# Optimization experiments

Hardware: AMD Instinct MI355X
Metric: run time of the kernel (lower is better)

The kernel has to match this reference:

```python
import jax, jax.numpy as jnp
import numpy as np

V = 30000   # vocab (from get_word_embedding default)
D = 640     # d_model
L = 6       # num_layers
H = 8       # num_heads
DH = D // H # head dim 80
FF = 4 * D  # ffn hidden 2560
BOS = 1
EOS = 2
LN_EPS = 1e-6


def _ln(x, s, b):
    m = x.mean(-1, keepdims=True)
    v = ((x - m) ** 2).mean(-1, keepdims=True)
    return (x - m) / jnp.sqrt(v + LN_EPS) * s + b


def _get_logits(tokens, seq_len, emb, Wq, bq, Wk, bk, Wv, bv, Wo, bo,
                ln1s, ln1b, W1, b1, W2, b2, ln2s, ln2b, lmW, lmb):
    # tokens: (B,S) int; seq_len: (B,) int
    B, S = tokens.shape
    h = emb[tokens]                                   # (B,S,D), no pos-enc / scaling in source
    look_ahead = jnp.triu(jnp.ones((S, S), jnp.float32), k=1)          # 1 = masked (TF-style)
    pad = (jnp.arange(S)[None, :] >= seq_len[:, None]).astype(jnp.float32)  # (B,S)
    mask = jnp.maximum(look_ahead[None, None, :, :], pad[:, None, None, :])  # (B,1,S,S)

    def layer(h, p):
        wq, bq_, wk, bk_, wv, bv_, wo, bo_, l1s, l1b, w1, b1_, w2, b2_, l2s, l2b = p
        q = (h @ wq + bq_).reshape(B, S, H, DH)
        k = (h @ wk + bk_).reshape(B, S, H, DH)
        v = (h @ wv + bv_).reshape(B, S, H, DH)
        scores = jnp.einsum('bqhd,bkhd->bhqk', q, k) / jnp.sqrt(jnp.float32(DH))
        scores = scores - mask * 1e9
        a = jax.nn.softmax(scores, axis=-1)
        o = jnp.einsum('bhqk,bkhd->bqhd', a, v).reshape(B, S, D) @ wo + bo_
        h = _ln(h + o, l1s, l1b)                      # post-LN residual
        f = jax.nn.relu(h @ w1 + b1_) @ w2 + b2_
        h = _ln(h + f, l2s, l2b)
        return h, None

    h, _ = jax.lax.scan(layer, h, (Wq, bq, Wk, bk, Wv, bv, Wo, bo,
                                   ln1s, ln1b, W1, b1, W2, b2, ln2s, ln2b))
    return h @ lmW + lmb                              # (B,S,V)


def setup_inputs() -> dict:
    key = jax.random.key(0)
    ks = jax.random.split(key, 12)
    std = 0.02

    def n(k, shape):
        return jax.random.normal(k, shape, jnp.float32) * std

    return {
        'initial_words': jax.random.randint(ks[0], (4, 8), 3, V, dtype=jnp.int32),
        'max_length': 32,
        'emb': n(ks[1], (V, D)),
        'Wq': n(ks[2], (L, D, D)), 'bq': jnp.zeros((L, D), jnp.float32),
        'Wk': n(ks[3], (L, D, D)), 'bk': jnp.zeros((L, D), jnp.float32),
        'Wv': n(ks[4], (L, D, D)), 'bv': jnp.zeros((L, D), jnp.float32),
        'Wo': n(ks[5], (L, D, D)), 'bo': jnp.zeros((L, D), jnp.float32),
        'ln1s': jnp.ones((L, D), jnp.float32), 'ln1b': jnp.zeros((L, D), jnp.float32),
        'W1': n(ks[6], (L, D, FF)), 'b1': jnp.zeros((L, FF), jnp.float32),
        'W2': n(ks[7], (L, FF, D)), 'b2': jnp.zeros((L, D), jnp.float32),
        'ln2s': jnp.ones((L, D), jnp.float32), 'ln2b': jnp.zeros((L, D), jnp.float32),
        'lmW': n(ks[8], (D, V)), 'lmb': jnp.zeros((V,), jnp.float32),
    }


def reference(initial_words, max_length, emb, Wq, bq, Wk, bk, Wv, bv, Wo, bo,
              ln1s, ln1b, W1, b1, W2, b2, ln2s, ln2b, lmW, lmb):
    B, init_len = initial_words.shape
    seq_len = jnp.full((B,), max_length, jnp.int32)
    S = max_length + 1  # BOS + max_length slots, as in the torch padding logic
    inp = (jnp.zeros((B, S), jnp.int32)
           .at[:, 0].set(BOS)
           .at[:, 1:1 + init_len].set(initial_words.astype(jnp.int32)))

    def cond(c):
        _inp, cl, tok = c
        return (cl + 1 <= max_length) & jnp.any(tok != EOS)

    def body(c):
        inp, cl, _tok = c
        logits = _get_logits(inp, seq_len, emb, Wq, bq, Wk, bk, Wv, bv, Wo, bo,
                             ln1s, ln1b, W1, b1, W2, b2, ln2s, ln2b, lmW, lmb)
        step_logits = jax.lax.dynamic_index_in_dim(logits, cl, axis=1, keepdims=False)
        tok = jnp.argmax(step_logits, axis=-1).astype(jnp.int32)
        inp = inp.at[:, cl + 1].set(tok)
        return (inp, cl + 1, tok)

    inp, _, _ = jax.lax.while_loop(
        cond, body,
        (inp, jnp.int32(init_len), jnp.full((B,), -100, jnp.int32)))
    return inp[:, 1:]
```

## Files before the change

kernel.cpp:

```cpp
#include <hip/hip_runtime.h>
#include <math.h>

#define B 4
#define SEQ 33
#define MAXLEN 32
#define D 640
#define NH 8
#define DH 80
#define NL 6
#define FF 2560
#define V 30000
#define INITLEN 8
#define NBLK 1024
#define NT 256
#define EOS_TOK 2
#define NPOS_P 9
#define NR_P 36
#define LM_NB 938

#define QKV_N 240
#define AW_B 240
#define AW_E 304
#define F1_B 304
#define F1_E 624
#define F2_B 624
#define F2_E 784

#define NFLAGS 1024
#define NSLOT 32
#define SLOT_U 16

#define VER(t,l) ((size_t)((t) * NL + (l)))

typedef float f4 __attribute__((ext_vector_type(4)));

struct Par {
  const int* iw;
  const float* emb;
  const float *Wq, *bq, *Wk, *bk, *Wv, *bv, *Wo, *bo;
  const float *ln1s, *ln1b, *W1, *b1, *W2, *b2, *ln2s, *ln2b, *lmW, *lmb;
  int* out;
};

__device__ __align__(256) float g_Kc[(size_t)NL * B * NH * SEQ * DH];
__device__ __align__(256) float g_Vc[(size_t)NL * B * NH * SEQ * DH];
__device__ __align__(256) float g_xv[(size_t)SEQ * NL * 2560];
__device__ __align__(256) float g_h1v[(size_t)SEQ * NL * 2560];
__device__ __align__(256) float g_qv[(size_t)SEQ * NL * 2560];
__device__ __align__(256) float g_opartv[(size_t)SEQ * NL * 20480];
__device__ __align__(256) float g_f1v[(size_t)SEQ * NL * 10240];
__device__ __align__(256) float g_f2v[(size_t)SEQ * NL * 5120];
__device__ __align__(256) float g_xlm[(size_t)SEQ * 2560];
__device__ __align__(256) int   g_tokv[SEQ * 64];
__device__ __align__(256) int   g_stopv[SEQ * 64];
__device__ float g_xp[NR_P * D];
__device__ float g_h1p[NR_P * D];
__device__ float g_qkvpP[(size_t)8 * 1920 * NR_P];
__device__ float g_qP[(size_t)NH * NR_P * DH];
__device__ float g_opartP[(size_t)NH * D * NR_P];
__device__ float g_f1pP[(size_t)8 * FF * NR_P];
__device__ float g_f2pP[(size_t)32 * D * NR_P];
__device__ unsigned long long g_keys[(size_t)NBLK * B];
__device__ int g_tokens[B * SEQ];
__device__ unsigned g_flags[(size_t)NFLAGS * NSLOT * SLOT_U];
__device__ unsigned g_arrive = 0;
__device__ unsigned g_gen = 0;

#define KCIDX(l,b,h,pos,j) (((((size_t)(l)*B+(b))*NH+(h))*SEQ+(pos))*DH+(j))

__device__ __forceinline__ float ldc(const float* p) {
  return __hip_atomic_load(p, __ATOMIC_RELAXED, __HIP_MEMORY_SCOPE_AGENT);
}
__device__ __forceinline__ void stc(float* p, float v) {
  __hip_atomic_store(p, v, __ATOMIC_RELAXED, __HIP_MEMORY_SCOPE_AGENT);
}
__device__ __forceinline__ int ldci(const int* p) {
  return __hip_atomic_load(p, __ATOMIC_RELAXED, __HIP_MEMORY_SCOPE_AGENT);
}
__device__ __forceinline__ void stci(int* p, int v) {
  __hip_atomic_store(p, v, __ATOMIC_RELAXED, __HIP_MEMORY_SCOPE_AGENT);
}
__device__ __forceinline__ void stcu64(unsigned long long* p, unsigned long long v) {
  __hip_atomic_store(p, v, __ATOMIC_RELAXED, __HIP_MEMORY_SCOPE_AGENT);
}
__device__ __forceinline__ void st4c(float* p, f4 v) {
  asm volatile("global_store_dwordx4 %0, %1, off sc1" :: "v"(p), "v"(v) : "memory");
}
__device__ __forceinline__ void ld4c_issue(f4& dst, const float* p) {
  asm volatile("global_load_dwordx4 %0, %1, off sc1" : "=v"(dst) : "v"(p) : "memory");
}
__device__ __forceinline__ void wait_vm() {
  asm volatile("s_waitcnt vmcnt(0)" ::: "memory");
  __builtin_amdgcn_sched_barrier(0);
}
__device__ __forceinline__ unsigned long long mk64(float lo, float hi) {
  return ((unsigned long long)__float_as_uint(hi) << 32) | (unsigned long long)__float_as_uint(lo);
}

__device__ __forceinline__ void gsync_full() {
  __syncthreads();
  if (threadIdx.x == 0) {
    __threadfence();
    unsigned g = __hip_atomic_load(&g_gen, __ATOMIC_SEQ_CST, __HIP_MEMORY_SCOPE_AGENT);
    unsigned old = __hip_atomic_fetch_add(&g_arrive, 1u, __ATOMIC_SEQ_CST, __HIP_MEMORY_SCOPE_AGENT);
    if (old == NBLK - 1u) {
      __hip_atomic_store(&g_arrive, 0u, __ATOMIC_SEQ_CST, __HIP_MEMORY_SCOPE_AGENT);
      __hip_atomic_fetch_add(&g_gen, 1u, __ATOMIC_SEQ_CST, __HIP_MEMORY_SCOPE_AGENT);
    } else {
      while (__hip_atomic_load(&g_gen, __ATOMIC_RELAXED, __HIP_MEMORY_SCOPE_AGENT) == g)
        __builtin_amdgcn_s_sleep(2);
    }
    __threadfence();
  }
  __syncthreads();
}

__device__ __forceinline__ void stage_done(int idx) {
  asm volatile("s_waitcnt vmcnt(0)" ::: "memory");
  __syncthreads();
  if (threadIdx.x == 0) {
    __hip_atomic_fetch_add(
        &g_flags[((size_t)idx * NSLOT + (blockIdx.x & (NSLOT - 1))) * SLOT_U],
        1u, __ATOMIC_RELAXED, __HIP_MEMORY_SCOPE_AGENT);
  }
}

__device__ __forceinline__ void stage_wait(int idx, unsigned cnt) {
  if (threadIdx.x < 64) {
    const unsigned* base = &g_flags[(size_t)idx * NSLOT * SLOT_U];
    int spins = 0;
    for (;;) {
      unsigned v = 0u;
      if (threadIdx.x < NSLOT)
        v = __hip_atomic_load(base + (size_t)threadIdx.x * SLOT_U,
                              __ATOMIC_RELAXED, __HIP_MEMORY_SCOPE_AGENT);
      #pragma unroll
      for (int o = 16; o > 0; o >>= 1) v += __shfl_down(v, o, 64);
      v = __shfl(v, 0, 64);
      if (v >= cnt) break;
      if (spins < 16)       __builtin_amdgcn_s_sleep(1);
      else if (spins < 128) __builtin_amdgcn_s_sleep(8);
      else                  __builtin_amdgcn_s_sleep(32);
      ++spins;
    }
  }
  __syncthreads();
  asm volatile("" ::: "memory");
}

__device__ __forceinline__ float bred_sum(float v, float* s_red) {
  #pragma unroll
  for (int o = 32; o > 0; o >>= 1) v += __shfl_down(v, o, 64);
  __syncthreads();
  if ((threadIdx.x & 63) == 0) s_red[threadIdx.x >> 6] = v;
  __syncthreads();
  return s_red[0] + s_red[1] + s_red[2] + s_red[3];
}

__device__ void ln_inplace(float* row, const float* gam, const float* bet, float* s_red) {
  float ps = 0.f;
  for (int d = threadIdx.x; d < D; d += NT) ps += row[d];
  const float m = bred_sum(ps, s_red) * (1.0f / 640.0f);
  float pv = 0.f;
  for (int d = threadIdx.x; d < D; d += NT) { float t = row[d] - m; pv += t * t; }
  const float var = bred_sum(pv, s_red) * (1.0f / 640.0f);
  const float rstd = 1.0f / sqrtf(var + 1e-6f);
  for (int d = threadIdx.x; d < D; d += NT)
    row[d] = (row[d] - m) * rstd * gam[d] + bet[d];
  __syncthreads();
}

__device__ __forceinline__ void ln_wave(float* s_x, const float* gam, const float* bet) {
  const int tid = threadIdx.x, w = tid >> 6, lane = tid & 63;
  float ps = 0.f;
  for (int i = lane; i < D; i += 64) ps += s_x[w * 640 + i];
  #pragma unroll
  for (int o = 32; o > 0; o >>= 1) ps += __shfl_xor(ps, o, 64);
  const float mean = ps * (1.0f / 640.0f);
  float pv = 0.f;
  for (int i = lane; i < D; i += 64) { float d = s_x[w * 640 + i] - mean; pv += d * d; }
  #pragma unroll
  for (int o = 32; o > 0; o >>= 1) pv += __shfl_xor(pv, o, 64);
  const float rstd = 1.0f / sqrtf(pv * (1.0f / 640.0f) + 1e-6f);
  for (int i = lane; i < D; i += 64)
    s_x[w * 640 + i] = (s_x[w * 640 + i] - mean) * rstd * gam[i] + bet[i];
}

__device__ __forceinline__ void build_x2w(const Par& p, int t, int lsrc, float* s_x) {
  const int tid = threadIdx.x, w = tid >> 6, lane = tid & 63;
  const size_t ver = VER(t, lsrc);
  const float* h1 = g_h1v + ver * 2560 + w * 640;
  const float* fa = g_f2v + ver * 5120 + w * 640;
  const float* fb = g_f2v + ver * 5120 + 2560 + w * 640;
  const float* b2 = p.b2 + (size_t)lsrc * D;
  for (int c4 = lane; c4 < 160; c4 += 64) {
    f4 a = *(const f4*)&h1[c4 * 4];
    f4 b = *(const f4*)&fa[c4 * 4];
    f4 c = *(const f4*)&fb[c4 * 4];
    const float* bb = b2 + c4 * 4;
    f4 s = { a.x + b.x + c.x + bb[0], a.y + b.y + c.y + bb[1],
             a.z + b.z + c.z + bb[2], a.w + b.w + c.w + bb[3] };
    *(f4*)&s_x[w * 640 + c4 * 4] = s;
  }
  ln_wave(s_x, p.ln2s + (size_t)lsrc * D, p.ln2b + (size_t)lsrc * D);
}


__device__ void st_QKV(const Par& p, int l, int t, float* s_x, float* s_t, float* s_r) {
  const int tid = threadIdx.x;
  const int cg = (blockIdx.x & 7) * 30 + (blockIdx.x >> 3);
  const int m = cg / 80, colm0 = (cg % 80) * 8;
  const int w = tid >> 6, lane = tid & 63;
  if (l == 0) {
    const int tok = g_tokv[t * 64 + w];
    for (int c4 = lane; c4 < 160; c4 += 64)
      *(f4*)&s_x[w * 640 + c4 * 4] = *(const f4*)&p.emb[(size_t)tok * D + c4 * 4];
  } else {
    build_x2w(p, t, l - 1, s_x);
  }
  __syncthreads();
  if (cg == 0) {
    const size_t xo = VER(t, l) * 2560;
    for (int i = tid; i < 640; i += NT)
      st4c(&g_xv[xo + (size_t)i * 4], *(f4*)&s_x[i * 4]);
  }
  const int ds = tid >> 3, c = tid & 7;
  const float* Wb = (m == 0 ? p.Wq : m == 1 ? p.Wk : p.Wv)
                    + (size_t)l * D * D + colm0 + c;
  float a0 = 0, a1 = 0, a2 = 0, a3 = 0;
  {
    float wv[20];
    #pragma unroll
    for (int j = 0; j < 20; ++j) wv[j] = Wb[(size_t)(ds + j * 32) * D];
    #pragma unroll
    for (int j = 0; j < 20; ++j) {
      const int dd = ds + j * 32;
      a0 = fmaf(s_x[dd],        wv[j], a0);
      a1 = fmaf(s_x[640 + dd],  wv[j], a1);
      a2 = fmaf(s_x[1280 + dd], wv[j], a2);
      a3 = fmaf(s_x[1920 + dd], wv[j], a3);
    }
  }
  { f4 av = { a0, a1, a2, a3 }; *(f4*)&s_t[c * 132 + ds * 4] = av; }
  __syncthreads();
  if (tid < 32) {
    const int c2 = tid >> 2, b = tid & 3;
    float v = 0.f;
    #pragma unroll
    for (int d2 = 0; d2 < 32; ++d2) v += s_t[c2 * 132 + d2 * 4 + b];
    v += (m == 0 ? p.bq : m == 1 ? p.bk : p.bv)[(size_t)l * D + colm0 + c2];
    s_r[c2 * 4 + b] = v;
  }
  __syncthreads();
  if (m == 0) {
    if (tid < 8) {
      f4 v = { s_r[tid * 4], s_r[tid * 4 + 1], s_r[tid * 4 + 2], s_r[tid * 4 + 3] };
      st4c(&g_qv[VER(t, l) * 2560 + (size_t)(colm0 + tid) * 4], v);
    }
  } else {
    const int h = colm0 / 80, j0 = colm0 % 80;
    if (tid < 8) {
      const int b = tid >> 1, cq4 = (tid & 1) * 4;
      f4 v = { s_r[(cq4+0)*4+b], s_r[(cq4+1)*4+b], s_r[(cq4+2)*4+b], s_r[(cq4+3)*4+b] };
      float* cache = (m == 1) ? g_Kc : g_Vc;
      st4c(&cache[KCIDX(l, b, h, t, j0 + cq4)], v);
    }
  }
}

__device__ void st_AW(const Par& p, int l, int t,
                      float* s_q, float* s_sc, float* s_o, float* s_wo) {
  const int idx = blockIdx.x - AW_B, h = idx >> 3, c = idx & 7, tid = threadIdx.x;
  const size_t qo = VER(t, l) * 2560;
  if (tid < 80) {
    f4 q = *(const f4*)&g_qv[qo + (size_t)(h * 80 + tid) * 4];
    s_q[tid] = q.x; s_q[80 + tid] = q.y; s_q[160 + tid] = q.z; s_q[240 + tid] = q.w;
  }
  __syncthreads();
  const int nk = t + 1;
  for (int task = tid; task < 4 * nk; task += NT) {
    const int b = task / nk, kp = task % nk;
    const float* qq = s_q + b * 80;
    const f4* kk = (const f4*)&g_Kc[KCIDX(l, b, h, kp, 0)];
    float sd = 0.f;
    #pragma unroll
    for (int j4 = 0; j4 < 20; ++j4) {
      f4 k4 = kk[j4];
      sd += qq[j4*4+0]*k4.x + qq[j4*4+1]*k4.y + qq[j4*4+2]*k4.z + qq[j4*4+3]*k4.w;
    }
    s_sc[b * 33 + kp] = sd / 8.94427190999915878564f;
  }
  __syncthreads();
  if (tid < 4) {
    const int b = tid;
    float m = -1e30f;
    for (int k = 0; k < nk; ++k) m = fmaxf(m, s_sc[b * 33 + k]);
    float sum = 0.f;
    for (int k = 0; k < nk; ++k) { float e = expf(s_sc[b * 33 + k] - m); s_sc[b * 33 + k] = e; sum += e; }
    s_sc[132 + b] = 1.0f / sum;
  }
  __syncthreads();
  if (tid < 80) {
    const int b = tid / 20, j4 = tid % 20;
    f4 acc = { 0.f, 0.f, 0.f, 0.f };
    for (int kp = 0; kp < nk; ++kp) {
      f4 v = *(const f4*)&g_Vc[KCIDX(l, b, h, kp, j4 * 4)];
      const float wgt = s_sc[b * 33 + kp];
      acc.x += wgt * v.x; acc.y += wgt * v.y; acc.z += wgt * v.z; acc.w += wgt * v.w;
    }
    const float r = s_sc[132 + b];
    f4 o = { acc.x * r, acc.y * r, acc.z * r, acc.w * r };
    *(f4*)&s_o[b * 80 + j4 * 4] = o;
  }
  __syncthreads();
  if (tid < 240) {
    const int j = tid % 80, sub = tid / 80;
    const int col = c * 80 + j;
    const int d0 = sub * 27, d1 = (sub == 2) ? 80 : d0 + 27;
    const float* Wo = p.Wo + (size_t)l * D * D + col;
    float a0 = 0, a1 = 0, a2 = 0, a3 = 0;
    #pragma unroll 9
    for (int dd = d0; dd < d1; ++dd) {
      const float w = Wo[(size_t)(h * 80 + dd) * D];
      a0 += s_o[0*80+dd] * w; a1 += s_o[80+dd] * w;
      a2 += s_o[160+dd] * w; a3 += s_o[240+dd] * w;
    }
    float* tp = s_wo + (j * 3 + sub) * 4;
    tp[0] = a0; tp[1] = a1; tp[2] = a2; tp[3] = a3;
  }
  __syncthreads();
  if (tid < 80) {
    const int b = tid / 20, cq = tid % 20;
    f4 v;
    #pragma unroll
    for (int i = 0; i < 4; ++i) {
      const int j = cq * 4 + i;
      v[i] = s_wo[(j*3+0)*4+b] + s_wo[(j*3+1)*4+b] + s_wo[(j*3+2)*4+b];
    }
    st4c(&g_opartv[VER(t, l) * 20480 + (size_t)(h * 4 + b) * 640 + c * 80 + cq * 4], v);
  }
}

__device__ void st_F1(const Par& p, int l, int t, float* s_x, float* s_t, float* s_r) {
  const int tid = threadIdx.x;
  const int raw = blockIdx.x - F1_B;
  const int cg = (raw & 7) * 40 + (raw >> 3);
  const int col0 = cg * 8;
  const size_t ver = VER(t, l);
  const int w = tid >> 6, lane = tid & 63;
  {
    const float* xv = g_xv + ver * 2560 + w * 640;
    const float* bo = p.bo + (size_t)l * D;
    for (int c4 = lane; c4 < 160; c4 += 64) {
      f4 a = *(const f4*)&xv[c4 * 4];
      const float* bb = bo + c4 * 4;
      a.x += bb[0]; a.y += bb[1]; a.z += bb[2]; a.w += bb[3];
      #pragma unroll
      for (int h = 0; h < 8; ++h) {
        f4 ov = *(const f4*)&g_opartv[ver * 20480 + (size_t)(h * 4 + w) * 640 + c4 * 4];
        a.x += ov.x; a.y += ov.y; a.z += ov.z; a.w += ov.w;
      }
      *(f4*)&s_x[w * 640 + c4 * 4] = a;
    }
    ln_wave(s_x, p.ln1s + (size_t)l * D, p.ln1b + (size_t)l * D);
  }
  __syncthreads();
  if (raw == 0) {
    for (int i = tid; i < 640; i += NT)
      st4c(&g_h1v[ver * 2560 + (size_t)i * 4], *(f4*)&s_x[i * 4]);
  }
  const int ds = tid >> 3, c = tid & 7;
  const float* Wb = p.W1 + (size_t)l * D * FF + col0 + c;
  float a0 = 0, a1 = 0, a2 = 0, a3 = 0;
  {
    float wv[20];
    #pragma unroll
    for (int j = 0; j < 20; ++j) wv[j] = Wb[(size_t)(ds + j * 32) * FF];
    #pragma unroll
    for (int j = 0; j < 20; ++j) {
      const int dd = ds + j * 32;
      a0 = fmaf(s_x[dd],        wv[j], a0);
      a1 = fmaf(s_x[640 + dd],  wv[j], a1);
      a2 = fmaf(s_x[1280 + dd], wv[j], a2);
      a3 = fmaf(s_x[1920 + dd], wv[j], a3);
    }
  }
  { f4 av = { a0, a1, a2, a3 }; *(f4*)&s_t[c * 132 + ds * 4] = av; }
  __syncthreads();
  if (tid < 32) {
    const int c2 = tid >> 2, b = tid & 3;
    float v = 0.f;
    #pragma unroll
    for (int d2 = 0; d2 < 32; ++d2) v += s_t[c2 * 132 + d2 * 4 + b];
    v += p.b1[(size_t)l * FF + col0 + c2];
    s_r[c2 * 4 + b] = fmaxf(v, 0.f);
  }
  __syncthreads();
  if (tid < 8) {
    const int b = tid >> 1, cq4 = (tid & 1) * 4;
    f4 v = { s_r[(cq4+0)*4+b], s_r[(cq4+1)*4+b], s_r[(cq4+2)*4+b], s_r[(cq4+3)*4+b] };
    st4c(&g_f1v[ver * 10240 + (size_t)b * 2560 + col0 + cq4], v);
  }
}

__device__ void st_F2(const Par& p, int l, int t, float* s_f, float* s_t, float* s_r) {
  const int idx = blockIdx.x - F2_B, tid = threadIdx.x;
  const int hf = idx / 80, craw = idx % 80;
  const int cg = (craw & 7) * 10 + (craw >> 3);
  const int col0 = cg * 8;
  const size_t ver = VER(t, l);
  #pragma unroll
  for (int i = 0; i < 5; ++i) {
    const int ii = tid + i * NT;
    const int b = ii / 320, fo = ii % 320;
    *(f4*)&s_f[b * 1280 + fo * 4] =
        *(const f4*)&g_f1v[ver * 10240 + (size_t)b * 2560 + hf * 1280 + fo * 4];
  }
  __syncthreads();
  const int ds = tid >> 3, c = tid & 7;
  const float* Wb = p.W2 + (size_t)l * FF * D + (size_t)hf * 1280 * D + col0 + c;
  float a0 = 0, a1 = 0, a2 = 0, a3 = 0;
  #pragma unroll
  for (int kb = 0; kb < 40; kb += 20) {
    float wv[20];
    #pragma unroll
    for (int j = 0; j < 20; ++j) wv[j] = Wb[(size_t)(ds + (kb + j) * 32) * D];
    #pragma unroll
    for (int j = 0; j < 20; ++j) {
      const int dl = ds + (kb + j) * 32;
      a0 = fmaf(s_f[dl],        wv[j], a0);
      a1 = fmaf(s_f[1280 + dl], wv[j], a1);
      a2 = fmaf(s_f[2560 + dl], wv[j], a2);
      a3 = fmaf(s_f[3840 + dl], wv[j], a3);
    }
  }
  { f4 av = { a0, a1, a2, a3 }; *(f4*)&s_t[c * 132 + ds * 4] = av; }
  __syncthreads();
  if (tid < 32) {
    const int c2 = tid >> 2, b = tid & 3;
    float v = 0.f;
    #pragma unroll
    for (int d2 = 0; d2 < 32; ++d2) v += s_t[c2 * 132 + d2 * 4 + b];
    s_r[c2 * 4 + b] = v;
  }
  __syncthreads();
  if (tid < 8) {
    const int b = tid >> 1, cq4 = (tid & 1) * 4;
    f4 v = { s_r[(cq4+0)*4+b], s_r[(cq4+1)*4+b], s_r[(cq4+2)*4+b], s_r[(cq4+3)*4+b] };
    st4c(&g_f2v[ver * 5120 + (size_t)(hf * 4 + b) * 640 + col0 + cq4], v);
  }
}

__device__ void st_LM(const Par& p, int t, int src, float* s_xf, float* s_part,
                      unsigned long long* s_key) {
  const int bid = blockIdx.x, tid = threadIdx.x;
  const int xcd = bid & 7, jj = bid >> 3;
  const int chunk = (xcd < 2 ? xcd * 118 : 236 + (xcd - 2) * 117) + jj;
  if (src == 0) {
    #pragma unroll
    for (int i = 0; i < 3; ++i) {
      const int idx = tid + i * NT;
      if (idx < 640) *(f4*)&s_xf[idx * 4] = *(const f4*)&g_xlm[(size_t)t * 2560 + (size_t)idx * 4];
    }
  } else {
    build_x2w(p, t, NL - 1, s_xf);
  }
  __syncthreads();
  const int sg = tid >> 5, cj = tid & 31;
  const int col = chunk * 32 + cj;
  float a0 = 0, a1 = 0, a2 = 0, a3 = 0;
  if (col < V) {
    const float* W = p.lmW + (size_t)sg * 80 * V + col;
    #pragma unroll
    for (int kb = 0; kb < 80; kb += 20) {
      float w[20];
      #pragma unroll
      for (int j = 0; j < 20; ++j) w[j] = W[(size_t)(kb + j) * V];
      #pragma unroll
      for (int j = 0; j < 20; ++j) {
        const int d = sg * 80 + kb + j;
        a0 = fmaf(s_xf[d],        w[j], a0);
        a1 = fmaf(s_xf[640 + d],  w[j], a1);
        a2 = fmaf(s_xf[1280 + d], w[j], a2);
        a3 = fmaf(s_xf[1920 + d], w[j], a3);
      }
    }
  }
  float* tp = s_part + (sg * 32 + cj) * 4;
  tp[0] = a0; tp[1] = a1; tp[2] = a2; tp[3] = a3;
  __syncthreads();
  if (tid < 128) {
    const int cj2 = tid >> 2, b = tid & 3, col2 = chunk * 32 + cj2;
    unsigned long long key = 0ull;
    if (col2 < V) {
      float a = p.lmb[col2];
      #pragma unroll
      for (int sg2 = 0; sg2 < 8; ++sg2) a += s_part[(sg2 * 32 + cj2) * 4 + b];
      unsigned u = __float_as_uint(a);
      u = (u & 0x80000000u) ? ~u : (u | 0x80000000u);
      key = ((unsigned long long)u << 32) | (unsigned)(V - col2);
    }
    s_key[cj2 * 4 + b] = key;
  }
  __syncthreads();
  if (tid < 4) {
    unsigned long long k0 = 0ull;
    for (int cj2 = 0; cj2 < 32; ++cj2) {
      const unsigned long long k = s_key[cj2 * 4 + tid];
      if (k > k0) k0 = k;
    }
    stcu64(&g_keys[(size_t)bid * B + tid], k0);
  }
}

__device__ void st_CTL(int t, unsigned long long* s_k64, int* s_ctl) {
  const int tid = threadIdx.x;
  const int i0 = tid, i1 = tid + NT, i2 = tid + 2 * NT, i3 = tid + 3 * NT;
  f4 z = { 0.f, 0.f, 0.f, 0.f };
  f4 ka0, kb0, ka1, kb1, ka2, kb2, ka3 = z, kb3 = z;
  ld4c_issue(ka0, (const float*)&g_keys[(size_t)i0 * 4]);
  ld4c_issue(kb0, (const float*)&g_keys[(size_t)i0 * 4 + 2]);
  ld4c_issue(ka1, (const float*)&g_keys[(size_t)i1 * 4]);
  ld4c_issue(kb1, (const float*)&g_keys[(size_t)i1 * 4 + 2]);
  ld4c_issue(ka2, (const float*)&g_keys[(size_t)i2 * 4]);
  ld4c_issue(kb2, (const float*)&g_keys[(size_t)i2 * 4 + 2]);
  if (i3 < LM_NB) {
    ld4c_issue(ka3, (const float*)&g_keys[(size_t)i3 * 4]);
    ld4c_issue(kb3, (const float*)&g_keys[(size_t)i3 * 4 + 2]);
  }
  wait_vm();
  unsigned long long m0 = mk64(ka0.x, ka0.y), m1 = mk64(ka0.z, ka0.w);
  unsigned long long m2 = mk64(kb0.x, kb0.y), m3 = mk64(kb0.z, kb0.w);
  { unsigned long long s;
    s = mk64(ka1.x,ka1.y); if (s>m0) m0=s;  s = mk64(ka1.z,ka1.w); if (s>m1) m1=s;
    s = mk64(kb1.x,kb1.y); if (s>m2) m2=s;  s = mk64(kb1.z,kb1.w); if (s>m3) m3=s;
    s = mk64(ka2.x,ka2.y); if (s>m0) m0=s;  s = mk64(ka2.z,ka2.w); if (s>m1) m1=s;
    s = mk64(kb2.x,kb2.y); if (s>m2) m2=s;  s = mk64(kb2.z,kb2.w); if (s>m3) m3=s;
    s = mk64(ka3.x,ka3.y); if (s>m0) m0=s;  s = mk64(ka3.z,ka3.w); if (s>m1) m1=s;
    s = mk64(kb3.x,kb3.y); if (s>m2) m2=s;  s = mk64(kb3.z,kb3.w); if (s>m3) m3=s;
  }
  #pragma unroll
  for (int o = 32; o > 0; o >>= 1) {
    unsigned long long s;
    s = __shfl_down(m0, o, 64); if (s > m0) m0 = s;
    s = __shfl_down(m1, o, 64); if (s > m1) m1 = s;
    s = __shfl_down(m2, o, 64); if (s > m2) m2 = s;
    s = __shfl_down(m3, o, 64); if (s > m3) m3 = s;
  }
  if ((tid & 63) == 0) {
    const int w = tid >> 6;
    s_k64[w * 4 + 0] = m0; s_k64[w * 4 + 1] = m1;
    s_k64[w * 4 + 2] = m2; s_k64[w * 4 + 3] = m3;
  }
  __syncthreads();
  if (tid == 0) {
    #pragma unroll
    for (int b = 0; b < B; ++b) {
      unsigned long long k0 = s_k64[b];
      #pragma unroll
      for (int w = 1; w < 4; ++w) if (s_k64[w * 4 + b] > k0) k0 = s_k64[w * 4 + b];
      const int tok = V - (int)(unsigned)(k0 & 0xFFFFFFFFull);
      stci(&g_tokens[b * SEQ + t + 1], tok);
      stci(&g_tokv[(t + 1) * 64 + b], tok);
      s_ctl[b] = tok;
    }
    int stop = (t == MAXLEN - 1) ? 1 : 0;
    if (s_ctl[0] == EOS_TOK && s_ctl[1] == EOS_TOK &&
        s_ctl[2] == EOS_TOK && s_ctl[3] == EOS_TOK) stop = 1;
    stci(&g_stopv[t * 64], stop);
  }
}


__device__ void st_Qp(const Par& p, int l, float* s_a) {
  const int idx = blockIdx.x, tid = threadIdx.x;
  const int h = idx / 24, rem = idx % 24, s = rem / 3, rg = rem % 3;
  const int r0 = rg * 12, d0 = s * 80;
  for (int i = tid; i < 960; i += NT) {
    const int ri = i / 80, dd = i % 80;
    s_a[i] = ldc(&g_xp[(r0 + ri) * D + d0 + dd]);
  }
  __syncthreads();
  if (tid < 240) {
    const int m = tid / 80, j = tid % 80, col = h * 80 + j;
    const float* W = (m == 0 ? p.Wq : m == 1 ? p.Wk : p.Wv) + (size_t)l * D * D + col;
    float acc[12];
    #pragma unroll
    for (int ri = 0; ri < 12; ++ri) acc[ri] = 0.f;
    for (int dd = 0; dd < 80; ++dd) {
      const float w = W[(size_t)(d0 + dd) * D];
      #pragma unroll
      for (int ri = 0; ri < 12; ++ri) acc[ri] += s_a[ri * 80 + dd] * w;
    }
    float* o = g_qkvpP + ((size_t)s * 1920 + m * 640 + col) * NR_P + r0;
    #pragma unroll
    for (int ri = 0; ri < 12; ++ri) stc(o + ri, acc[ri]);
  }
}

__device__ void st_AWp1(const Par& p, int l) {
  const int idx = blockIdx.x - 192, h = idx >> 2, c = idx & 3, tid = threadIdx.x;
  for (int pp = c; pp < NPOS_P; pp += 4) {
    for (int task = tid; task < 960; task += NT) {
      const int m = task / 320, rem = task % 320, j = rem >> 2, b = rem & 3;
      const int r = pp * 4 + b;
      const int col = m * 640 + h * 80 + j;
      const float* q = g_qkvpP + (size_t)col * NR_P + r;
      float a = 0.f;
      #pragma unroll
      for (int s = 0; s < 8; ++s) a += ldc(q + (size_t)s * 1920 * NR_P);
      a += (m == 0 ? p.bq : m == 1 ? p.bk : p.bv)[(size_t)l * D + h * 80 + j];
      if (m == 0)      stc(&g_qP[((size_t)h * NR_P + r) * DH + j], a);
      else if (m == 1) stc(&g_Kc[KCIDX(l, b, h, pp, j)], a);
      else             stc(&g_Vc[KCIDX(l, b, h, pp, j)], a);
    }
  }
}

__device__ void st_AWp2(const Par& p, int l, float* s_a, float* s_b, float* s_c) {
  const int idx = blockIdx.x - 224, h = idx >> 2, rg = idx & 3, tid = threadIdx.x;
  const int r0 = rg * 9;
  for (int i = tid; i < 720; i += NT) {
    const int ri = i / 80, j = i % 80;
    s_a[i] = ldc(&g_qP[((size_t)h * NR_P + r0 + ri) * DH + j]);
  }
  __syncthreads();
  for (int task = tid; task < 81; task += NT) {
    const int ri = task / 9, kp = task % 9;
    const int r = r0 + ri, pos = r >> 2, b = r & 3;
    if (kp <= pos) {
      const float* kk = g_Kc + KCIDX(l, b, h, kp, 0);
      const float* qq = s_a + ri * 80;
      float sd = 0.f;
      for (int j = 0; j < 80; ++j) sd += qq[j] * ldc(kk + j);
      s_c[ri * 9 + kp] = sd / 8.94427190999915878564f;
    }
  }
  __syncthreads();
  if (tid < 9) {
    const int ri = tid, r = r0 + ri, pos = r >> 2;
    float m = -1e30f;
    for (int k = 0; k <= pos; ++k) m = fmaxf(m, s_c[ri * 9 + k]);
    float sum = 0.f;
    for (int k = 0; k <= pos; ++k) { float e = expf(s_c[ri * 9 + k] - m); s_c[ri * 9 + k] = e; sum += e; }
    s_c[81 + ri] = 1.0f / sum;
  }
  __syncthreads();
  for (int task = tid; task < 720; task += NT) {
    const int ri = task / 80, j = task % 80;
    const int r = r0 + ri, pos = r >> 2, b = r & 3;
    float acc = 0.f;
    for (int kp = 0; kp <= pos; ++kp)
      acc += s_c[ri * 9 + kp] * ldc(&g_Vc[KCIDX(l, b, h, kp, j)]);
    s_b[ri * 80 + j] = acc * s_c[81 + ri];
  }
  __syncthreads();
  if (tid < 160) {
    for (int pass = 0; pass < 4; ++pass) {
      const int col = pass * 160 + tid;
      const float* Wo = p.Wo + (size_t)l * D * D + col;
      float acc[9];
      #pragma unroll
      for (int ri = 0; ri < 9; ++ri) acc[ri] = 0.f;
      for (int dd = 0; dd < 80; ++dd) {
        const float w = Wo[(size_t)(h * 80 + dd) * D];
        #pragma unroll
        for (int ri = 0; ri < 9; ++ri) acc[ri] += s_b[ri * 80 + dd] * w;
      }
      #pragma unroll
      for (int ri = 0; ri < 9; ++ri)
        stc(&g_opartP[((size_t)h * D + col) * NR_P + r0 + ri], acc[ri]);
    }
  }
}

__device__ void st_RFp(const Par& p, int l, float* s_row, float* s_red) {
  const int r = blockIdx.x, tid = threadIdx.x;
  for (int col = tid; col < D; col += NT) {
    float a = ldc(&g_xp[r * D + col]) + p.bo[(size_t)l * D + col];
    #pragma unroll
    for (int h = 0; h < 8; ++h) a += ldc(&g_opartP[((size_t)h * D + col) * NR_P + r]);
    s_row[col] = a;
  }
  __syncthreads();
  ln_inplace(s_row, p.ln1s + (size_t)l * D, p.ln1b + (size_t)l * D, s_red);
  for (int col = tid; col < D; col += NT) stc(&g_h1p[r * D + col], s_row[col]);
}

__device__ void st_F1p(const Par& p, int l, float* s_a) {
  const int idx = blockIdx.x, tid = threadIdx.x;
  const int s = idx / 30, rem = idx % 30, cg = rem / 3, rg = rem % 3;
  const int r0 = rg * 12, d0 = s * 80;
  for (int i = tid; i < 960; i += NT) {
    const int ri = i / 80, dd = i % 80;
    s_a[i] = ldc(&g_h1p[(r0 + ri) * D + d0 + dd]);
  }
  __syncthreads();
  const int col = cg * 256 + tid;
  const float* W = p.W1 + (size_t)l * D * FF + col;
  float acc[12];
  #pragma unroll
  for (int ri = 0; ri < 12; ++ri) acc[ri] = 0.f;
  for (int dd = 0; dd < 80; ++dd) {
    const float w = W[(size_t)(d0 + dd) * FF];
    #pragma unroll
    for (int ri = 0; ri < 12; ++ri) acc[ri] += s_a[ri * 80 + dd] * w;
  }
  float* o = g_f1pP + ((size_t)s * FF + col) * NR_P + r0;
  #pragma unroll
  for (int ri = 0; ri < 12; ++ri) stc(o + ri, acc[ri]);
}

__device__ void st_F2p(const Par& p, int l, float* s_c) {
  const int idx = blockIdx.x - 240, c = idx / 3, rg = idx % 3, tid = threadIdx.x;
  const int r0 = rg * 12;
  for (int task = tid; task < 960; task += NT) {
    const int ri = task / 80, fj = task % 80;
    const int fcol = c * 80 + fj;
    const float* pp = g_f1pP + (size_t)fcol * NR_P + r0 + ri;
    float a = 0.f;
    #pragma unroll
    for (int s = 0; s < 8; ++s) a += ldc(pp + (size_t)s * FF * NR_P);
    a += p.b1[(size_t)l * FF + fcol];
    s_c[ri * 80 + fj] = fmaxf(a, 0.f);
  }
  __syncthreads();
  for (int pass = 0; pass < 3; ++pass) {
    const int col = pass * 256 + tid;
    if (col < D) {
      const float* W = p.W2 + (size_t)l * FF * D + col;
      float acc[12];
      #pragma unroll
      for (int ri = 0; ri < 12; ++ri) acc[ri] = 0.f;
      for (int fj = 0; fj < 80; ++fj) {
        const float w = W[(size_t)(c * 80 + fj) * D];
        #pragma unroll
        for (int ri = 0; ri < 12; ++ri) acc[ri] += s_c[ri * 80 + fj] * w;
      }
      float* o = g_f2pP + ((size_t)c * D + col) * NR_P + r0;
      #pragma unroll
      for (int ri = 0; ri < 12; ++ri) stc(o + ri, acc[ri]);
    }
  }
}

__device__ void st_RQp(const Par& p, int l, float* s_row, float* s_red) {
  const int r = blockIdx.x, tid = threadIdx.x;
  for (int col = tid; col < D; col += NT) {
    float a = ldc(&g_h1p[r * D + col]) + p.b2[(size_t)l * D + col];
    #pragma unroll 8
    for (int c = 0; c < 32; ++c) a += ldc(&g_f2pP[((size_t)c * D + col) * NR_P + r]);
    s_row[col] = a;
  }
  __syncthreads();
  ln_inplace(s_row, p.ln2s + (size_t)l * D, p.ln2b + (size_t)l * D, s_red);
  for (int col = tid; col < D; col += NT) stc(&g_xp[r * D + col], s_row[col]);
}

__device__ void st_RLp(const Par& p, float* s_row, float* s_red) {
  const int b = blockIdx.x, r = 32 + b, tid = threadIdx.x;
  for (int col = tid; col < D; col += NT) {
    float a = ldc(&g_h1p[r * D + col]) + p.b2[(size_t)(NL - 1) * D + col];
    #pragma unroll 8
    for (int c = 0; c < 32; ++c) a += ldc(&g_f2pP[((size_t)c * D + col) * NR_P + r]);
    s_row[col] = a;
  }
  __syncthreads();
  ln_inplace(s_row, p.ln2s + (size_t)(NL - 1) * D, p.ln2b + (size_t)(NL - 1) * D, s_red);
  for (int col = tid; col < D; col += NT)
    stc(&g_xlm[(size_t)INITLEN * 2560 + (size_t)b * 640 + col], s_row[col]);
}

__global__ __launch_bounds__(NT, 4) void tfgen(Par p) {
  __shared__ float s_pool[6400];
  __shared__ float s_red[8];
  __shared__ unsigned long long s_key[128];
  __shared__ int s_ctl[8];

  const int bid = blockIdx.x, tid = threadIdx.x;
  int ep = 0;

  {
    unsigned* f = g_flags + (size_t)bid * NSLOT * SLOT_U;
    for (int i = tid; i < NSLOT * SLOT_U; i += NT) f[i] = 0u;
  }
  if (bid < NR_P) {
    const int pos = bid >> 2, b = bid & 3;
    const int tk = (pos == 0) ? 1 : p.iw[b * INITLEN + pos - 1];
    for (int d = tid; d < D; d += NT) stc(&g_xp[bid * D + d], p.emb[(size_t)tk * D + d]);
  }
  if (bid == NBLK - 1) {
    for (int i = tid; i < B * SEQ; i += NT) {
      const int b = i / SEQ, pos = i % SEQ;
      int tk = 0;
      if (pos == 0) tk = 1;
      else if (pos <= INITLEN) tk = p.iw[b * INITLEN + pos - 1];
      stci(&g_tokens[i], tk);
    }
  }
  gsync_full();

  float* ps_x  = s_pool;
  float* ps_a  = s_pool + 2560;
  float* ps_b  = s_pool + 3584;
  float* ps_c  = s_pool + 4352;
  int eRQ = -1, eF2last = -1;
  for (int l = 0; l < NL; ++l) {
    const int eQ = ep++;
    if (bid < 192) { if (l > 0) stage_wait(eRQ, 36); st_Qp(p, l, ps_a); stage_done(eQ); }
    const int eA1 = ep++;
    if (bid >= 192 && bid < 224) { stage_wait(eQ, 192); st_AWp1(p, l); stage_done(eA1); }
    const int eA2 = ep++;
    if (bid >= 224 && bid < 256) { stage_wait(eA1, 32); st_AWp2(p, l, ps_a, ps_b, ps_c); stage_done(eA2); }
    const int eRF = ep++;
    if (bid < NR_P) { stage_wait(eA2, 32); st_RFp(p, l, ps_x, s_red); stage_done(eRF); }
    const int eF1 = ep++;
    if (bid < 240) { stage_wait(eRF, 36); st_F1p(p, l, ps_a); stage_done(eF1); }
    const int eF2 = ep++;
    if (bid >= 240 && bid < 336) { stage_wait(eF1, 240); st_F2p(p, l, ps_c); stage_done(eF2); }
    eF2last = eF2;
    if (l < NL - 1) {
      eRQ = ep++;
      if (bid < NR_P) { stage_wait(eF2, 96); st_RQp(p, l, ps_x, s_red); stage_done(eRQ); }
    }
  }

  for (int t = INITLEN;; ++t) {
    int eCTL;
    if (t == INITLEN) {
      const int eRLp = ep++;
      if (bid < 4) { stage_wait(eF2last, 96); st_RLp(p, s_pool, s_red); stage_done(eRLp); }
      const int eLM = ep++;
      if (bid < LM_NB) { stage_wait(eRLp, 4); st_LM(p, t, 0, s_pool, s_pool + 2560, s_key); stage_done(eLM); }
      eCTL = ep++;
      if (bid == NBLK - 1) { stage_wait(eLM, LM_NB); st_CTL(t, s_key, s_ctl); stage_done(eCTL); }
    } else {
      int eF2s = -1;
      for (int l = 0; l < NL; ++l) {
        const int eQKV = ep++;
        if (bid < QKV_N) {
          if (l > 0) stage_wait(eF2s, 160);
          st_QKV(p, l, t, s_pool, s_pool + 2560, s_pool + 3648);
          stage_done(eQKV);
        }
        const int eAW = ep++;
        if (bid >= AW_B && bid < AW_E) {
          stage_wait(eQKV, QKV_N);
          st_AW(p, l, t, s_pool, s_pool + 320, s_pool + 480, s_pool + 800);
          stage_done(eAW);
        }
        const int eF1 = ep++;
        if (bid >= F1_B && bid < F1_E) {
          stage_wait(eAW, 64);
          st_F1(p, l, t, s_pool, s_pool + 2560, s_pool + 3648);
          stage_done(eF1);
        }
        eF2s = ep++;
        if (bid >= F2_B && bid < F2_E) {
          stage_wait(eF1, 320);
          st_F2(p, l, t, s_pool, s_pool + 5120, s_pool + 6208);
          stage_done(eF2s);
        }
      }
      const int eLM = ep++;
      if (bid < LM_NB) { stage_wait(eF2s, 160); st_LM(p, t, 1, s_pool, s_pool + 2560, s_key); stage_done(eLM); }
      eCTL = ep++;
      if (bid == NBLK - 1) { stage_wait(eLM, LM_NB); st_CTL(t, s_key, s_ctl); stage_done(eCTL); }
    }
    stage_wait(eCTL, 1);
    if (g_stopv[t * 64]) break;
  }

  if (bid == 0) {
    for (int i = tid; i < B * MAXLEN; i += NT) {
      const int b = i >> 5, j = i & 31;
      p.out[i] = ldci(&g_tokens[b * SEQ + j + 1]);
    }
  }
}

extern "C" void kernel_launch(void* const* d_in, const int* in_sizes, int n_in,
                              void* d_out, int out_size, void* d_ws, size_t ws_size,
                              hipStream_t stream)
{
  (void)in_sizes; (void)n_in; (void)out_size; (void)d_ws; (void)ws_size;
  Par p;
  p.iw   = (const int*)  d_in[0];
  p.emb  = (const float*)d_in[2];
  p.Wq   = (const float*)d_in[3];  p.bq   = (const float*)d_in[4];
  p.Wk   = (const float*)d_in[5];  p.bk   = (const float*)d_in[6];
  p.Wv   = (const float*)d_in[7];  p.bv   = (const float*)d_in[8];
  p.Wo   = (const float*)d_in[9];  p.bo   = (const float*)d_in[10];
  p.ln1s = (const float*)d_in[11]; p.ln1b = (const float*)d_in[12];
  p.W1   = (const float*)d_in[13]; p.b1   = (const float*)d_in[14];
  p.W2   = (const float*)d_in[15]; p.b2   = (const float*)d_in[16];
  p.ln2s = (const float*)d_in[17]; p.ln2b = (const float*)d_in[18];
  p.lmW  = (const float*)d_in[19]; p.lmb  = (const float*)d_in[20];
  p.out  = (int*)d_out;

  void* args[] = { (void*)&p };
  hipError_t err = hipLaunchCooperativeKernel((const void*)tfgen, dim3(NBLK), dim3(NT),
                                              args, 0, stream);
  if (err != hipSuccess) {
    hipLaunchKernelGGL(tfgen, dim3(NBLK), dim3(NT), 0, stream, p);
  }
}
```

Before: 16.34 ms.

## Prefetch each stage's weight slice into cache while waiting on dependencies

Before each block spins on its stage dependency, it reads the exact weight slice it will later use (QKV, Wo, W1, W2, LM head) and discards the sum through an empty asm sink. This warms L2/MALL so the real stage after the wait finds its weights in cache, hiding HBM latency behind synchronization idle time. The cost is duplicated global loads and possible cache thrashing if the total weight footprint exceeds cache capacity, especially for the large LM head.

New measurement: 17.02 ms. 4.2% more time.

```diff
diff --git a/kernel.cpp b/kernel.cpp
--- a/kernel.cpp
+++ b/kernel.cpp
@@ -96,6 +96,7 @@
 __device__ __forceinline__ unsigned long long mk64(float lo, float hi) {
   return ((unsigned long long)__float_as_uint(hi) << 32) | (unsigned long long)__float_as_uint(lo);
 }
+__device__ __forceinline__ void keep(float x) { asm volatile("" :: "v"(x)); }
 
 __device__ __forceinline__ void gsync_full() {
   __syncthreads();
@@ -203,6 +204,73 @@
     *(f4*)&s_x[w * 640 + c4 * 4] = s;
   }
   ln_wave(s_x, p.ln2s + (size_t)lsrc * D, p.ln2b + (size_t)lsrc * D);
+}
+
+
+__device__ void pf_QKV(const Par& p, int l) {
+  const int tid = threadIdx.x;
+  const int cg = (blockIdx.x & 7) * 30 + (blockIdx.x >> 3);
+  const int m = cg / 80, colm0 = (cg % 80) * 8;
+  const int ds = tid >> 3, c = tid & 7;
+  const float* Wb = (m == 0 ? p.Wq : m == 1 ? p.Wk : p.Wv)
+                    + (size_t)l * D * D + colm0 + c;
+  float s = 0.f;
+  #pragma unroll
+  for (int j = 0; j < 20; ++j) s += Wb[(size_t)(ds + j * 32) * D];
+  keep(s);
+}
+
+__device__ void pf_AW(const Par& p, int l) {
+  const int idx = blockIdx.x - AW_B, h = idx >> 3, c = idx & 7, tid = threadIdx.x;
+  if (tid < 240) {
+    const int j = tid % 80, sub = tid / 80;
+    const int col = c * 80 + j;
+    const int d0 = sub * 27, d1 = (sub == 2) ? 80 : d0 + 27;
+    const float* Wo = p.Wo + (size_t)l * D * D + col;
+    float s = 0.f;
+    for (int dd = d0; dd < d1; ++dd) s += Wo[(size_t)(h * 80 + dd) * D];
+    keep(s);
+  }
+}
+
+__device__ void pf_F1(const Par& p, int l) {
+  const int tid = threadIdx.x;
+  const int raw = blockIdx.x - F1_B;
+  const int cg = (raw & 7) * 40 + (raw >> 3);
+  const int col0 = cg * 8;
+  const int ds = tid >> 3, c = tid & 7;
+  const float* Wb = p.W1 + (size_t)l * D * FF + col0 + c;
+  float s = 0.f;
+  #pragma unroll
+  for (int j = 0; j < 20; ++j) s += Wb[(size_t)(ds + j * 32) * FF];
+  keep(s);
+}
+
+__device__ void pf_F2(const Par& p, int l) {
+  const int idx = blockIdx.x - F2_B, tid = threadIdx.x;
+  const int hf = idx / 80, craw = idx % 80;
+  const int cg = (craw & 7) * 10 + (craw >> 3);
+  const int col0 = cg * 8;
+  const int ds = tid >> 3, c = tid & 7;
+  const float* Wb = p.W2 + (size_t)l * FF * D + (size_t)hf * 1280 * D + col0 + c;
+  float s = 0.f;
+  #pragma unroll
+  for (int kb = 0; kb < 40; ++kb) s += Wb[(size_t)(ds + kb * 32) * D];
+  keep(s);
+}
+
+__device__ void pf_LM(const Par& p) {
+  const int bid = blockIdx.x, tid = threadIdx.x;
+  const int xcd = bid & 7, jj = bid >> 3;
+  const int chunk = (xcd < 2 ? xcd * 118 : 236 + (xcd - 2) * 117) + jj;
+  const int sg = tid >> 5, cj = tid & 31;
+  const int col = chunk * 32 + cj;
+  if (col < V) {
+    const float* W = p.lmW + (size_t)sg * 80 * V + col;
+    float s = 0.f;
+    for (int kb = 0; kb < 80; ++kb) s += W[(size_t)kb * V];
+    keep(s);
+  }
 }
 
 
@@ -831,7 +899,7 @@
       const int eRLp = ep++;
       if (bid < 4) { stage_wait(eF2last, 96); st_RLp(p, s_pool, s_red); stage_done(eRLp); }
       const int eLM = ep++;
-      if (bid < LM_NB) { stage_wait(eRLp, 4); st_LM(p, t, 0, s_pool, s_pool + 2560, s_key); stage_done(eLM); }
+      if (bid < LM_NB) { pf_LM(p); stage_wait(eRLp, 4); st_LM(p, t, 0, s_pool, s_pool + 2560, s_key); stage_done(eLM); }
       eCTL = ep++;
       if (bid == NBLK - 1) { stage_wait(eLM, LM_NB); st_CTL(t, s_key, s_ctl); stage_done(eCTL); }
     } else {
@@ -839,34 +907,43 @@
       for (int l = 0; l < NL; ++l) {
         const int eQKV = ep++;
         if (bid < QKV_N) {
-          if (l > 0) stage_wait(eF2s, 160);
+          if (l > 0) { pf_QKV(p, l); stage_wait(eF2s, 160); }
           st_QKV(p, l, t, s_pool, s_pool + 2560, s_pool + 3648);
           stage_done(eQKV);
         }
         const int eAW = ep++;
         if (bid >= AW_B && bid < AW_E) {
+          pf_AW(p, l);
           stage_wait(eQKV, QKV_N);
           st_AW(p, l, t, s_pool, s_pool + 320, s_pool + 480, s_pool + 800);
           stage_done(eAW);
         }
         const int eF1 = ep++;
         if (bid >= F1_B && bid < F1_E) {
+          pf_F1(p, l);
           stage_wait(eAW, 64);
           st_F1(p, l, t, s_pool, s_pool + 2560, s_pool + 3648);
           stage_done(eF1);
         }
         eF2s = ep++;
         if (bid >= F2_B && bid < F2_E) {
+          pf_F2(p, l);
           stage_wait(eF1, 320);
           st_F2(p, l, t, s_pool, s_pool + 5120, s_pool + 6208);
           stage_done(eF2s);
         }
       }
       const int eLM = ep++;
-      if (bid < LM_NB) { stage_wait(eF2s, 160); st_LM(p, t, 1, s_pool, s_pool + 2560, s_key); stage_done(eLM); }
+      if (bid < LM_NB) {
+        pf_LM(p);
+        stage_wait(eF2s, 160);
+        st_LM(p, t, 1, s_pool, s_pool + 2560, s_key);
+        stage_done(eLM);
+      }
       eCTL = ep++;
       if (bid == NBLK - 1) { stage_wait(eLM, LM_NB); st_CTL(t, s_key, s_ctl); stage_done(eCTL); }
     }
+    if (bid < QKV_N) pf_QKV(p, 0);
     stage_wait(eCTL, 1);
     if (g_stopv[t * 64]) break;
   }
```
